# Kernel tuning notes

Hardware: AMD Instinct MI355X
Metric: run time of the kernel (lower is better)

Reference implementation:

```python
import jax, jax.numpy as jnp
import numpy as np

WIN = 5
EPS = 1e-05


def box_sum(x, win=WIN):
    """3D box-filter window sum, SAME padding (pad=win//2), via separable 1D convs.
    Mathematically identical to F.conv3d(x, ones(1,1,win,win,win), padding=win//2).
    x: [N, C, D, H, W]
    """
    pad = win // 2
    for ax in range(3):  # D, H, W
        kshape = [1, 1, 1, 1, 1]
        kshape[2 + ax] = win
        k = jnp.ones(kshape, x.dtype)
        pads = [(0, 0), (0, 0), (0, 0)]
        pads[ax] = (pad, pad)
        x = jax.lax.conv_general_dilated(
            x, k, window_strides=(1, 1, 1), padding=pads,
            dimension_numbers=('NCDHW', 'OIDHW', 'NCDHW'))
    return x


def setup_inputs() -> dict:
    key = jax.random.key(0)
    k1, k2 = jax.random.split(key)
    shape = (2, 1, 160, 192, 192)
    I = jax.random.normal(k1, shape, dtype=jnp.float32)
    J = jax.random.normal(k2, shape, dtype=jnp.float32)
    return {"I": I, "J": J}


def reference(I, J):
    V = float(WIN ** 3)  # window voxel count
    I_sum = box_sum(I)
    J_sum = box_sum(J)
    I2_sum = box_sum(I * I)
    J2_sum = box_sum(J * J)
    IJ_sum = box_sum(I * J)

    u_I = I_sum / V
    u_J = J_sum / V
    cross = IJ_sum - u_J * I_sum - u_I * J_sum + u_I * u_J * V
    I_var = I2_sum - 2.0 * u_I * I_sum + u_I * u_I * V
    J_var = J2_sum - 2.0 * u_J * J_sum + u_J * u_J * V
    cc = cross * cross / (I_var * J_var + EPS)
    # single channel: avg over channels is identity; loss = -mean(cc)
    return -1.0 * jnp.mean(cc)
```

## Files before the change

### kernel.cpp

```cpp
#include <hip/hip_runtime.h>


namespace {
constexpr int Wd = 192, Hd = 192, Dd = 160;
constexpr int SH = 192;
constexpr int SD = 192 * 192;
constexpr long SN = (long)SD * Dd;
constexpr int CD = 6;
constexpr int NCHUNK = 27;
constexpr int TROW = 72;
constexpr int TILEF = 2 * 20 * TROW;
constexpr float INV_V = 1.0f / 125.0f;
constexpr float EPSf = 1e-5f;

__device__ __forceinline__ void wslide(const float h[8], float o[4]) {
  float s0 = h[0] + h[1] + h[2] + h[3] + h[4];
  float s1 = s0 - h[0] + h[5];
  float s2 = s1 - h[1] + h[6];
  float s3 = s2 - h[2] + h[7];
  o[0] = s0; o[1] = s1; o[2] = s2; o[3] = s3;
}

__device__ __forceinline__ void gl_lds16(const float* g, float* l) {
  __builtin_amdgcn_global_load_lds(
      (const __attribute__((address_space(1))) void*)g,
      (__attribute__((address_space(3))) void*)l, 16, 0, 0);
}
}

__global__ __launch_bounds__(256) void ncc_fused(const float* __restrict__ I,
                                                 const float* __restrict__ Jv,
                                                 float* __restrict__ out) {
  __shared__ float tile[2][TILEF];
  __shared__ float red[4];

  const int tid = threadIdx.x;
  const int tx = tid & 15;
  const int ty = tid >> 4;
  const int wbase = blockIdx.x * 64;
  const int hbase = blockIdx.y * 16;
  const int n  = blockIdx.z / NCHUNK;
  const int d_lo = (blockIdx.z % NCHUNK) * CD;

  const float* Ib = I  + (long)n * SN;
  const float* Jb = Jv + (long)n * SN;

  const int wave = tid >> 6, lane = tid & 63;
  const int arr = wave >> 1;
  const float* gsrc = arr ? Jb : Ib;
  int goff[3]; int loff[3]; bool on[3];
  #pragma unroll
  for (int r = 0; r < 3; ++r) {
    const int seg = wave * 180 + r * 64 + lane;
    on[r] = (r < 2) || (lane < 52);
    const int rem = seg - arr * 360;
    const int row = rem / 18, c16 = rem % 18;
    const int hh = hbase + row - 2;
    const int hc = min(max(hh, 0), Hd - 1);
    const int gw = wbase - 4 + c16 * 4;
    const int gc = min(max(gw, 0), Wd - 4);
    goff[r] = hc * SH + gc;
    loff[r] = seg * 4;
  }

  {
    const int s0 = d_lo - 2;
    if (s0 >= 0 && s0 < Dd) {
      const float* base = gsrc + (long)s0 * SD;
      #pragma unroll
      for (int r = 0; r < 3; ++r) if (on[r]) gl_lds16(base + goff[r], &tile[0][loff[r]]);
    }
  }
  __syncthreads();

  const bool zl = (wbase == 0)   && (tx == 0);
  const bool zr = (wbase == 128) && (tx == 15);

  float ring[5][5][4];
  float acc = 0.0f;

  constexpr int T = CD + 4;
  for (int t0 = 0; t0 < T; t0 += 5) {
    #pragma unroll
    for (int p = 0; p < 5; ++p) {
      const int t = t0 + p;
      const int s = d_lo - 2 + t;

      {
        const int sn = s + 1;
        if ((t + 1) < T && sn >= 0 && sn < Dd) {
          const float* base = gsrc + (long)sn * SD;
          float* dst = &tile[(t + 1) & 1][0];
          #pragma unroll
          for (int r = 0; r < 3; ++r) if (on[r]) gl_lds16(base + goff[r], dst + loff[r]);
        }
      }

      float hsI[8], hsJ[8], hsII[8], hsJJ[8], hsIJ[8];
      #pragma unroll
      for (int c = 0; c < 8; ++c) {
        hsI[c] = 0.f; hsJ[c] = 0.f; hsII[c] = 0.f; hsJJ[c] = 0.f; hsIJ[c] = 0.f;
      }
      if (s >= 0 && s < Dd) {
        const float* bufc = &tile[t & 1][0];
        #pragma unroll
        for (int dh = 0; dh < 5; ++dh) {
          const int rrow = ty + dh;
          const int hh = hbase + rrow - 2;
          if (hh >= 0 && hh < Hd) {
            const float* pa = bufc + rrow * TROW + 4 * tx;
            const float* pb = pa + 20 * TROW;
            float a[12], b[12];
            ((float4*)a)[0] = ((const float4*)pa)[0];
            ((float4*)a)[1] = ((const float4*)pa)[1];
            ((float4*)a)[2] = ((const float4*)pa)[2];
            ((float4*)b)[0] = ((const float4*)pb)[0];
            ((float4*)b)[1] = ((const float4*)pb)[1];
            ((float4*)b)[2] = ((const float4*)pb)[2];
            if (zl) { a[2] = 0.f; a[3] = 0.f; b[2] = 0.f; b[3] = 0.f; }
            if (zr) { a[8] = 0.f; a[9] = 0.f; b[8] = 0.f; b[9] = 0.f; }
            #pragma unroll
            for (int c = 0; c < 8; ++c) {
              const float x = a[c + 2], y = b[c + 2];
              hsI[c]  += x;
              hsJ[c]  += y;
              hsII[c] = fmaf(x, x, hsII[c]);
              hsJJ[c] = fmaf(y, y, hsJJ[c]);
              hsIJ[c] = fmaf(x, y, hsIJ[c]);
            }
          }
        }
      }

      wslide(hsI,  ring[p][0]);
      wslide(hsJ,  ring[p][1]);
      wslide(hsII, ring[p][2]);
      wslide(hsJJ, ring[p][3]);
      wslide(hsIJ, ring[p][4]);

      const int d = d_lo + t - 4;
      if (t >= 4 && d < Dd) {
        #pragma unroll
        for (int k = 0; k < 4; ++k) {
          float SI = 0.f, SJ = 0.f, SII = 0.f, SJJ = 0.f, SIJ = 0.f;
          #pragma unroll
          for (int q = 0; q < 5; ++q) {
            SI  += ring[q][0][k];
            SJ  += ring[q][1][k];
            SII += ring[q][2][k];
            SJJ += ring[q][3][k];
            SIJ += ring[q][4][k];
          }
          const float cross = SIJ - SI * SJ * INV_V;
          const float vI    = SII - SI * SI * INV_V;
          const float vJ    = SJJ - SJ * SJ * INV_V;
          acc += cross * cross / (vI * vJ + EPSf);
        }
      }

      __syncthreads();
    }
  }

  #pragma unroll
  for (int off = 32; off > 0; off >>= 1) acc += __shfl_xor(acc, off, 64);
  if ((tid & 63) == 0) red[tid >> 6] = acc;
  __syncthreads();
  if (tid == 0) {
    const float total = red[0] + red[1] + red[2] + red[3];
    atomicAdd(out, total * (-1.0f / 11796480.0f));
  }
}

extern "C" void kernel_launch(void* const* d_in, const int* in_sizes, int n_in,
                              void* d_out, int out_size, void* d_ws, size_t ws_size,
                              hipStream_t stream) {
  const float* I = (const float*)d_in[0];
  const float* J = (const float*)d_in[1];
  float* out = (float*)d_out;
  hipMemsetAsync(out, 0, sizeof(float), stream);
  dim3 grid(3, 12, 2 * NCHUNK);
  ncc_fused<<<grid, 256, 0, stream>>>(I, J, out);
}
```

Before: 165.0 us.

## Replace LDS tile staging with direct global loads and longer depth chunks

Removes the double-buffered LDS tile filled by global_load_lds, along with the per-slice __syncthreads, and has each thread read its 5 rows of I and J straight from global memory (relying on L1/L2 for reuse). The depth chunk grows from 6 to 16 slices with 10 chunks, which lowers the halo recompute overhead but also shrinks the grid. Interior waves get a branch-free path with no per-row bounds checks. The trade-off is more redundant global/L1 traffic, since each row is read by several threads, and fewer blocks to hide latency.

```diff
diff --git a/kernel.cpp b/kernel.cpp
--- a/kernel.cpp
+++ b/kernel.cpp
@@ -6,10 +6,8 @@
 constexpr int SH = 192;
 constexpr int SD = 192 * 192;
 constexpr long SN = (long)SD * Dd;
-constexpr int CD = 6;
-constexpr int NCHUNK = 27;
-constexpr int TROW = 72;
-constexpr int TILEF = 2 * 20 * TROW;
+constexpr int CD = 16;
+constexpr int NCHUNK = 10;
 constexpr float INV_V = 1.0f / 125.0f;
 constexpr float EPSf = 1e-5f;
 
@@ -20,61 +18,42 @@
   float s3 = s2 - h[2] + h[7];
   o[0] = s0; o[1] = s1; o[2] = s2; o[3] = s3;
 }
-
-__device__ __forceinline__ void gl_lds16(const float* g, float* l) {
-  __builtin_amdgcn_global_load_lds(
-      (const __attribute__((address_space(1))) void*)g,
-      (__attribute__((address_space(3))) void*)l, 16, 0, 0);
-}
 }
 
 __global__ __launch_bounds__(256) void ncc_fused(const float* __restrict__ I,
                                                  const float* __restrict__ Jv,
                                                  float* __restrict__ out) {
-  __shared__ float tile[2][TILEF];
   __shared__ float red[4];
 
-  const int tid = threadIdx.x;
-  const int tx = tid & 15;
-  const int ty = tid >> 4;
+  const int tid  = threadIdx.x;
+  const int lane = tid & 63, wave = tid >> 6;
+  const int tx   = lane & 15;
+  const int tyw  = lane >> 4;
   const int wbase = blockIdx.x * 64;
   const int hbase = blockIdx.y * 16;
-  const int n  = blockIdx.z / NCHUNK;
+  const int n   = blockIdx.z / NCHUNK;
   const int d_lo = (blockIdx.z % NCHUNK) * CD;
+  const int hw0 = hbase + 4 * wave - 2;
+  const bool interior = (hw0 >= 0) && (hw0 + 7 < Hd);
 
   const float* Ib = I  + (long)n * SN;
   const float* Jb = Jv + (long)n * SN;
 
-  const int wave = tid >> 6, lane = tid & 63;
-  const int arr = wave >> 1;
-  const float* gsrc = arr ? Jb : Ib;
-  int goff[3]; int loff[3]; bool on[3];
-  #pragma unroll
-  for (int r = 0; r < 3; ++r) {
-    const int seg = wave * 180 + r * 64 + lane;
-    on[r] = (r < 2) || (lane < 52);
-    const int rem = seg - arr * 360;
-    const int row = rem / 18, c16 = rem % 18;
-    const int hh = hbase + row - 2;
-    const int hc = min(max(hh, 0), Hd - 1);
-    const int gw = wbase - 4 + c16 * 4;
-    const int gc = min(max(gw, 0), Wd - 4);
-    goff[r] = hc * SH + gc;
-    loff[r] = seg * 4;
-  }
-
-  {
-    const int s0 = d_lo - 2;
-    if (s0 >= 0 && s0 < Dd) {
-      const float* base = gsrc + (long)s0 * SD;
-      #pragma unroll
-      for (int r = 0; r < 3; ++r) if (on[r]) gl_lds16(base + goff[r], &tile[0][loff[r]]);
-    }
-  }
-  __syncthreads();
-
+  const int w0 = wbase + 4 * tx;
+  const int c0 = max(w0 - 4, 0);
+  const int c1 = w0;
+  const int c2 = min(w0 + 8, Wd - 4);
   const bool zl = (wbase == 0)   && (tx == 0);
   const bool zr = (wbase == 128) && (tx == 15);
+
+  int rcI[5][3]; bool rowok[5];
+  #pragma unroll
+  for (int dh = 0; dh < 5; ++dh) {
+    const int hh = hw0 + tyw + dh;
+    rowok[dh] = (hh >= 0) && (hh < Hd);
+    const int ro = min(max(hh, 0), Hd - 1) * SH;
+    rcI[dh][0] = ro + c0; rcI[dh][1] = ro + c1; rcI[dh][2] = ro + c2;
+  }
 
   float ring[5][5][4];
   float acc = 0.0f;
@@ -86,39 +65,41 @@
       const int t = t0 + p;
       const int s = d_lo - 2 + t;
 
-      {
-        const int sn = s + 1;
-        if ((t + 1) < T && sn >= 0 && sn < Dd) {
-          const float* base = gsrc + (long)sn * SD;
-          float* dst = &tile[(t + 1) & 1][0];
+      float hsI[8], hsJ[8], hsII[8], hsJJ[8], hsIJ[8];
+      if (s >= 0 && s < Dd) {
+        const float* pI = Ib + (long)s * SD;
+        const float* pJ = Jb + (long)s * SD;
+        if (interior) {
+          {
+            const int* rc = rcI[0];
+            float a[12], b[12];
+            ((float4*)a)[0] = *(const float4*)(pI + rc[0]);
+            ((float4*)a)[1] = *(const float4*)(pI + rc[1]);
+            ((float4*)a)[2] = *(const float4*)(pI + rc[2]);
+            ((float4*)b)[0] = *(const float4*)(pJ + rc[0]);
+            ((float4*)b)[1] = *(const float4*)(pJ + rc[1]);
+            ((float4*)b)[2] = *(const float4*)(pJ + rc[2]);
+            if (zl) { a[2]=0.f; a[3]=0.f; b[2]=0.f; b[3]=0.f; }
+            if (zr) { a[8]=0.f; a[9]=0.f; b[8]=0.f; b[9]=0.f; }
+            #pragma unroll
+            for (int c = 0; c < 8; ++c) {
+              const float x = a[c + 2], y = b[c + 2];
+              hsI[c] = x; hsJ[c] = y;
+              hsII[c] = x * x; hsJJ[c] = y * y; hsIJ[c] = x * y;
+            }
+          }
           #pragma unroll
-          for (int r = 0; r < 3; ++r) if (on[r]) gl_lds16(base + goff[r], dst + loff[r]);
-        }
-      }
-
-      float hsI[8], hsJ[8], hsII[8], hsJJ[8], hsIJ[8];
-      #pragma unroll
-      for (int c = 0; c < 8; ++c) {
-        hsI[c] = 0.f; hsJ[c] = 0.f; hsII[c] = 0.f; hsJJ[c] = 0.f; hsIJ[c] = 0.f;
-      }
-      if (s >= 0 && s < Dd) {
-        const float* bufc = &tile[t & 1][0];
-        #pragma unroll
-        for (int dh = 0; dh < 5; ++dh) {
-          const int rrow = ty + dh;
-          const int hh = hbase + rrow - 2;
-          if (hh >= 0 && hh < Hd) {
-            const float* pa = bufc + rrow * TROW + 4 * tx;
-            const float* pb = pa + 20 * TROW;
+          for (int dh = 1; dh < 5; ++dh) {
+            const int* rc = rcI[dh];
             float a[12], b[12];
-            ((float4*)a)[0] = ((const float4*)pa)[0];
-            ((float4*)a)[1] = ((const float4*)pa)[1];
-            ((float4*)a)[2] = ((const float4*)pa)[2];
-            ((float4*)b)[0] = ((const float4*)pb)[0];
-            ((float4*)b)[1] = ((const float4*)pb)[1];
-            ((float4*)b)[2] = ((const float4*)pb)[2];
-            if (zl) { a[2] = 0.f; a[3] = 0.f; b[2] = 0.f; b[3] = 0.f; }
-            if (zr) { a[8] = 0.f; a[9] = 0.f; b[8] = 0.f; b[9] = 0.f; }
+            ((float4*)a)[0] = *(const float4*)(pI + rc[0]);
+            ((float4*)a)[1] = *(const float4*)(pI + rc[1]);
+            ((float4*)a)[2] = *(const float4*)(pI + rc[2]);
+            ((float4*)b)[0] = *(const float4*)(pJ + rc[0]);
+            ((float4*)b)[1] = *(const float4*)(pJ + rc[1]);
+            ((float4*)b)[2] = *(const float4*)(pJ + rc[2]);
+            if (zl) { a[2]=0.f; a[3]=0.f; b[2]=0.f; b[3]=0.f; }
+            if (zr) { a[8]=0.f; a[9]=0.f; b[8]=0.f; b[9]=0.f; }
             #pragma unroll
             for (int c = 0; c < 8; ++c) {
               const float x = a[c + 2], y = b[c + 2];
@@ -129,6 +110,40 @@
               hsIJ[c] = fmaf(x, y, hsIJ[c]);
             }
           }
+        } else {
+          #pragma unroll
+          for (int c = 0; c < 8; ++c) {
+            hsI[c] = 0.f; hsJ[c] = 0.f; hsII[c] = 0.f; hsJJ[c] = 0.f; hsIJ[c] = 0.f;
+          }
+          #pragma unroll
+          for (int dh = 0; dh < 5; ++dh) {
+            if (rowok[dh]) {
+              const int* rc = rcI[dh];
+              float a[12], b[12];
+              ((float4*)a)[0] = *(const float4*)(pI + rc[0]);
+              ((float4*)a)[1] = *(const float4*)(pI + rc[1]);
+              ((float4*)a)[2] = *(const float4*)(pI + rc[2]);
+              ((float4*)b)[0] = *(const float4*)(pJ + rc[0]);
+              ((float4*)b)[1] = *(const float4*)(pJ + rc[1]);
+              ((float4*)b)[2] = *(const float4*)(pJ + rc[2]);
+              if (zl) { a[2]=0.f; a[3]=0.f; b[2]=0.f; b[3]=0.f; }
+              if (zr) { a[8]=0.f; a[9]=0.f; b[8]=0.f; b[9]=0.f; }
+              #pragma unroll
+              for (int c = 0; c < 8; ++c) {
+                const float x = a[c + 2], y = b[c + 2];
+                hsI[c]  += x;
+                hsJ[c]  += y;
+                hsII[c] = fmaf(x, x, hsII[c]);
+                hsJJ[c] = fmaf(y, y, hsJJ[c]);
+                hsIJ[c] = fmaf(x, y, hsIJ[c]);
+              }
+            }
+          }
+        }
+      } else {
+        #pragma unroll
+        for (int c = 0; c < 8; ++c) {
+          hsI[c] = 0.f; hsJ[c] = 0.f; hsII[c] = 0.f; hsJJ[c] = 0.f; hsIJ[c] = 0.f;
         }
       }
 
@@ -157,14 +172,12 @@
           acc += cross * cross / (vI * vJ + EPSf);
         }
       }
-
-      __syncthreads();
     }
   }
 
   #pragma unroll
   for (int off = 32; off > 0; off >>= 1) acc += __shfl_xor(acc, off, 64);
-  if ((tid & 63) == 0) red[tid >> 6] = acc;
+  if (lane == 0) red[wave] = acc;
   __syncthreads();
   if (tid == 0) {
     const float total = red[0] + red[1] + red[2] + red[3];
```

Result: slower. 195.2 us (+18.3%).
